# Optimization experiments

Hardware: AMD Instinct MI355X
Metric: run time of the kernel (lower is better)

Reference implementation:

```python
import jax, jax.numpy as jnp
import numpy as np
from jax import lax

B, L, H, V, INNER = 16, 2048, 512, 32000, 8
LR = 0.01
EPS = 1e-5
STD = 0.02


def setup_inputs() -> dict:
    key = jax.random.key(0)
    ks = jax.random.split(key, 14)
    n = lambda k, shape: (jax.random.normal(k, shape, dtype=jnp.float32) * STD)
    return {
        'seq': jax.random.randint(ks[0], (B, L), 0, V, dtype=jnp.int64),
        'embed': n(ks[1], (V, H)),
        'enc_w1': n(ks[2], (2 * H, H)), 'enc_b1': jnp.zeros((2 * H,), jnp.float32),
        'enc_w2': n(ks[3], (H, 2 * H)), 'enc_b2': jnp.zeros((H,), jnp.float32),
        'ln_w': jnp.ones((H,), jnp.float32), 'ln_b': jnp.zeros((H,), jnp.float32),
        'mlp_w1': n(ks[4], (INNER, H)), 'mlp_b1': jnp.zeros((INNER,), jnp.float32),
        'mlp_w2': n(ks[5], (H, INNER)), 'mlp_b2': jnp.zeros((H,), jnp.float32),
        'out_w': n(ks[6], (V, H)), 'out_b': jnp.zeros((V,), jnp.float32),
    }


def _encoder(seq, embed, enc_w1, enc_b1, enc_w2, enc_b2, ln_w, ln_b):
    h = embed[seq]                                        # [B,L,H]
    ff = jax.nn.relu(h @ enc_w1.T + enc_b1) @ enc_w2.T + enc_b2
    x = h + ff
    mu = jnp.mean(x, axis=-1, keepdims=True)
    var = jnp.mean(jnp.square(x - mu), axis=-1, keepdims=True)  # biased, as torch LayerNorm
    return (x - mu) * lax.rsqrt(var + EPS) * ln_w + ln_b


def _inner_mlp(w1, b1, w2, b2, x):
    return w2 @ jax.nn.relu(w1 @ x + b1) + b2


def _ttt_contexts(hidden, mlp_w1, mlp_b1, mlp_w2, mlp_b2):
    # torch detaches hidden and copies base_mlp weights: no grads flow here
    hidden = lax.stop_gradient(hidden)
    p0 = tuple(lax.stop_gradient(p) for p in (mlp_w1, mlp_b1, mlp_w2, mlp_b2))
    ts = np.arange(0, L - 3, 2)                           # 1023 sequential steps
    keys = hidden[:, ts]                                  # [B,T,H]
    vals = hidden[:, ts + 1]                              # [B,T,H]
    query = hidden[:, -1]                                 # [B,H]

    def step(p, kv):
        w1, b1, w2, b2 = p
        k, v = kv
        def loss(w1, b1, w2, b2):
            pred = _inner_mlp(w1, b1, w2, b2, k)
            return jnp.mean(jnp.square(pred - v))
        g1, gb1, g2, gb2 = jax.grad(loss, argnums=(0, 1, 2, 3))(w1, b1, w2, b2)
        return (w1 - LR * g1, b1 - LR * gb1, w2 - LR * g2, b2 - LR * gb2), None

    def run(kb, vb, qb):
        (w1, b1, w2, b2), _ = lax.scan(step, p0, (kb, vb))
        return _inner_mlp(w1, b1, w2, b2, qb)

    return jax.vmap(run)(keys, vals, query)               # [B,H]


def reference(seq, embed, enc_w1, enc_b1, enc_w2, enc_b2, ln_w, ln_b,
              mlp_w1, mlp_b1, mlp_w2, mlp_b2, out_w, out_b):
    hidden = _encoder(seq, embed, enc_w1, enc_b1, enc_w2, enc_b2, ln_w, ln_b)
    ctx = _ttt_contexts(hidden, mlp_w1, mlp_b1, mlp_w2, mlp_b2)
    return ctx @ out_w.T + out_b                          # [B,V]
```

## Files before the change

### kernel.cpp

```cpp
#include <hip/hip_runtime.h>

#define GAS __attribute__((address_space(1)))
#define LAS __attribute__((address_space(3)))

typedef __attribute__((ext_vector_type(8))) short bf16x8;
typedef __attribute__((ext_vector_type(4))) float f32x4;
typedef __attribute__((ext_vector_type(2))) float f32x2;

static constexpr int Bb = 16, Ll = 2048, Hh = 512, Vv = 32000, H2 = 1024;
static constexpr int Mtot = Bb * Ll;
static constexpr float LRc = 0.01f, EPSc = 1e-5f;

static constexpr size_t OFF_X    = 0;
static constexpr size_t OFF_EBF  = OFF_X   + (size_t)Mtot * Hh * 4;
static constexpr size_t OFF_W1BF = OFF_EBF + (size_t)Vv * Hh * 2;
static constexpr size_t OFF_W2BF = OFF_W1BF + (size_t)H2 * Hh * 2;
static constexpr size_t OFF_CTX  = OFF_W2BF + (size_t)Hh * H2 * 2;
static constexpr size_t OFF_FF1  = OFF_CTX + (size_t)Bb * Hh * 4;

__device__ inline unsigned short f2bf(float f) {
  unsigned u = __float_as_uint(f);
  return (unsigned short)((u + 0x7fffu + ((u >> 16) & 1u)) >> 16);
}

__device__ inline f32x2 pk_fma(f32x2 a, f32x2 b, f32x2 c) {
  f32x2 d;
  asm("v_pk_fma_f32 %0, %1, %2, %3" : "=v"(d) : "v"(a), "v"(b), "v"(c));
  return d;
}

#define DPP_ADD(ctrl)                                                        \
  {                                                                          \
    int t_ = __builtin_amdgcn_update_dpp(0, v_, ctrl, 0xf, 0xf, true);       \
    v_ = __float_as_int(__int_as_float(v_) + __int_as_float(t_));            \
  }
__device__ inline float wsum_bcast(float x) {
  int v_ = __float_as_int(x);
  DPP_ADD(0x111)
  DPP_ADD(0x112)
  DPP_ADD(0x114)
  DPP_ADD(0x118)
  DPP_ADD(0x142)
  DPP_ADD(0x143)
  return __int_as_float(__builtin_amdgcn_readlane(v_, 63));
}

__global__ __launch_bounds__(256) void cvt_bf16_kernel(const float* __restrict__ src,
                                                       unsigned short* __restrict__ dst, int n8) {
  int stride = gridDim.x * blockDim.x;
  for (int i = blockIdx.x * blockDim.x + threadIdx.x; i < n8; i += stride) {
    const float4* p = (const float4*)(src + (size_t)i * 8);
    float4 a = p[0], b = p[1];
    uint4 o;
    o.x = f2bf(a.x) | ((unsigned)f2bf(a.y) << 16);
    o.y = f2bf(a.z) | ((unsigned)f2bf(a.w) << 16);
    o.z = f2bf(b.x) | ((unsigned)f2bf(b.y) << 16);
    o.w = f2bf(b.z) | ((unsigned)f2bf(b.w) << 16);
    *(uint4*)(dst + (size_t)i * 8) = o;
  }
}

template <int KTOT, bool GATHER, bool RELUOUT>
__global__ __launch_bounds__(256) void gemm_bt(const unsigned short* __restrict__ Abase,
                                               const int* __restrict__ seq, int seq_off,
                                               const unsigned short* __restrict__ Bmat,
                                               const float* __restrict__ bias,
                                               unsigned short* __restrict__ outb,
                                               float* __restrict__ outf,
                                               int out_row_off, int ldout) {
  __shared__ unsigned short As[128 * 32];
  __shared__ unsigned short Bs[128 * 32];
  __shared__ unsigned long long aoff[128];
  const int tid = threadIdx.x;
  const int m0 = blockIdx.x * 128, n0 = blockIdx.y * 128;

  if (tid < 128) {
    long long r;
    if (GATHER) r = (long long)seq[seq_off + m0 + tid] * KTOT;
    else        r = (long long)(m0 + tid) * KTOT;
    aoff[tid] = (unsigned long long)r;
  }
  __syncthreads();

  const int srow = tid >> 2;
  const int scol = (tid & 3) * 8;
  const int wave = tid >> 6;
  const int lane = tid & 63;
  const int wr = wave >> 1, wc = wave & 1;
  const int fr = lane & 15;
  const int fk = (lane >> 4) * 8;

  f32x4 acc[4][4] = {};

  for (int k0 = 0; k0 < KTOT; k0 += 32) {
#pragma unroll
    for (int i = 0; i < 2; ++i) {
      const unsigned short* ga = Abase + aoff[i * 64 + srow] + k0 + scol;
      __builtin_amdgcn_global_load_lds((const GAS void*)ga,
          (LAS void*)((char*)As + i * 4096 + wave * 1024), 16, 0, 0);
      const unsigned short* gb = Bmat + (size_t)(n0 + i * 64 + srow) * KTOT + k0 + scol;
      __builtin_amdgcn_global_load_lds((const GAS void*)gb,
          (LAS void*)((char*)Bs + i * 4096 + wave * 1024), 16, 0, 0);
    }
    __syncthreads();
    bf16x8 af[4], bfr[4];
#pragma unroll
    for (int m = 0; m < 4; ++m)
      af[m] = *(const bf16x8*)&As[(wr * 64 + m * 16 + fr) * 32 + fk];
#pragma unroll
    for (int n = 0; n < 4; ++n)
      bfr[n] = *(const bf16x8*)&Bs[(wc * 64 + n * 16 + fr) * 32 + fk];
#pragma unroll
    for (int m = 0; m < 4; ++m)
#pragma unroll
      for (int n = 0; n < 4; ++n)
        acc[m][n] = __builtin_amdgcn_mfma_f32_16x16x32_bf16(af[m], bfr[n], acc[m][n], 0, 0, 0);
    __syncthreads();
  }

  float bv[4];
#pragma unroll
  for (int n = 0; n < 4; ++n) bv[n] = bias[n0 + wc * 64 + n * 16 + fr];
#pragma unroll
  for (int m = 0; m < 4; ++m) {
#pragma unroll
    for (int n = 0; n < 4; ++n) {
#pragma unroll
      for (int j = 0; j < 4; ++j) {
        int rl = wr * 64 + m * 16 + ((lane >> 4) << 2) + j;
        int col = n0 + wc * 64 + n * 16 + fr;
        float v = acc[m][n][j] + bv[n];
        size_t off = (size_t)(out_row_off + m0 + rl) * ldout + col;
        if (RELUOUT) { v = fmaxf(v, 0.f); outb[off] = f2bf(v); }
        else outf[off] = v;
      }
    }
  }
}

__global__ __launch_bounds__(256) void ln_kernel(float* __restrict__ xbuf,
                                                 const float* __restrict__ embed,
                                                 const int* __restrict__ seq,
                                                 const float* __restrict__ lnw,
                                                 const float* __restrict__ lnb) {
  int row = blockIdx.x * 4 + (threadIdx.x >> 6);
  int lane = threadIdx.x & 63;
  int c = lane * 8;
  int s = seq[row];
  float* xr = xbuf + (size_t)row * Hh;
  const float* hr = embed + (size_t)s * Hh;
  float4 f0 = *(const float4*)(xr + c), f1 = *(const float4*)(xr + c + 4);
  float4 h0 = *(const float4*)(hr + c), h1 = *(const float4*)(hr + c + 4);
  float x[8] = {f0.x + h0.x, f0.y + h0.y, f0.z + h0.z, f0.w + h0.w,
                f1.x + h1.x, f1.y + h1.y, f1.z + h1.z, f1.w + h1.w};
  float sm = 0.f, sq = 0.f;
#pragma unroll
  for (int u = 0; u < 8; ++u) { sm += x[u]; sq += x[u] * x[u]; }
#pragma unroll
  for (int m = 1; m < 64; m <<= 1) { sm += __shfl_xor(sm, m, 64); sq += __shfl_xor(sq, m, 64); }
  float mu = sm * (1.f / 512.f);
  float var = sq * (1.f / 512.f) - mu * mu;
  float rs = rsqrtf(var + EPSc);
  float y[8];
#pragma unroll
  for (int u = 0; u < 8; ++u) y[u] = (x[u] - mu) * rs * lnw[c + u] + lnb[c + u];
  *(float4*)(xr + c) = make_float4(y[0], y[1], y[2], y[3]);
  *(float4*)(xr + c + 4) = make_float4(y[4], y[5], y[6], y[7]);
}

__global__ __launch_bounds__(64, 1) void ttt_kernel(const float* __restrict__ hidden,
                                                    const float* __restrict__ w1_0,
                                                    const float* __restrict__ b1_0,
                                                    const float* __restrict__ w2_0,
                                                    const float* __restrict__ b2_0,
                                                    float* __restrict__ ctx) {
  const int b = blockIdx.x;
  const int l = threadIdx.x;
  const int c0 = l * 8;
  const float* hb = hidden + (size_t)b * Ll * Hh;
  const float scale = 2.0f / 512.0f;

  f32x2 W1v[8][4];
  f32x2 W2v[8][4];
  float B1[8], B2[8];
#pragma unroll
  for (int j = 0; j < 8; ++j) {
    float4 a = *(const float4*)(w1_0 + (size_t)j * Hh + c0);
    float4 d = *(const float4*)(w1_0 + (size_t)j * Hh + c0 + 4);
    W1v[j][0] = f32x2{a.x, a.y}; W1v[j][1] = f32x2{a.z, a.w};
    W1v[j][2] = f32x2{d.x, d.y}; W1v[j][3] = f32x2{d.z, d.w};
    B1[j] = b1_0[j];
  }
#pragma unroll
  for (int u = 0; u < 8; ++u) {
    float4 a = *(const float4*)(w2_0 + (size_t)(c0 + u) * 8);
    float4 d = *(const float4*)(w2_0 + (size_t)(c0 + u) * 8 + 4);
    W2v[u][0] = f32x2{a.x, a.y}; W2v[u][1] = f32x2{a.z, a.w};
    W2v[u][2] = f32x2{d.x, d.y}; W2v[u][3] = f32x2{d.z, d.w};
  }
  {
    float4 e = *(const float4*)(b2_0 + c0);
    float4 f = *(const float4*)(b2_0 + c0 + 4);
    B2[0] = e.x; B2[1] = e.y; B2[2] = e.z; B2[3] = e.w;
    B2[4] = f.x; B2[5] = f.y; B2[6] = f.z; B2[7] = f.w;
  }

  f32x2 Kc[4];
  float Vs[8];
  const float* pk = hb + c0;
  const float* pv = hb + Hh + c0;
  {
    float4 a = *(const float4*)pk, d = *(const float4*)(pk + 4);
    Kc[0] = f32x2{a.x, a.y}; Kc[1] = f32x2{a.z, a.w};
    Kc[2] = f32x2{d.x, d.y}; Kc[3] = f32x2{d.z, d.w};
    float4 e = *(const float4*)pv, f = *(const float4*)(pv + 4);
    Vs[0] = e.x; Vs[1] = e.y; Vs[2] = e.z; Vs[3] = e.w;
    Vs[4] = f.x; Vs[5] = f.y; Vs[6] = f.z; Vs[7] = f.w;
  }

#pragma unroll 2
  for (int t = 0; t < 1023; ++t) {
    float4 ka, kb, va, vb;
    const bool pre = (t < 1022);
    if (pre) {
      ka = *(const float4*)(pk + 1024); kb = *(const float4*)(pk + 1028);
      va = *(const float4*)(pv + 1024); vb = *(const float4*)(pv + 1028);
    }

    float z[8], h[8];
#pragma unroll
    for (int j = 0; j < 8; ++j) {
      f32x2 acc = {0.f, 0.f};
#pragma unroll
      for (int p = 0; p < 4; ++p) acc = pk_fma(W1v[j][p], Kc[p], acc);
      float s = wsum_bcast(acc.x + acc.y);
      z[j] = s + B1[j];
      h[j] = fmaxf(z[j], 0.f);
    }
    f32x2 h2[4];
#pragma unroll
    for (int p = 0; p < 4; ++p) h2[p] = f32x2{h[2 * p], h[2 * p + 1]};

    float d_[8];
    f32x2 dd[8];
#pragma unroll
    for (int u = 0; u < 8; ++u) {
      f32x2 acc = {0.f, 0.f};
#pragma unroll
      for (int p = 0; p < 4; ++p) acc = pk_fma(W2v[u][p], h2[p], acc);
      float pred = acc.x + acc.y + B2[u];
      float dv = (pred - Vs[u]) * scale;
      d_[u] = dv;
      dd[u] = f32x2{dv, dv};
    }

    f32x2 dhp[4] = {{0.f, 0.f}, {0.f, 0.f}, {0.f, 0.f}, {0.f, 0.f}};
#pragma unroll
    for (int u = 0; u < 8; ++u)
#pragma unroll
      for (int p = 0; p < 4; ++p) dhp[p] = pk_fma(W2v[u][p], dd[u], dhp[p]);
    float dz[8];
#pragma unroll
    for (int p = 0; p < 4; ++p) {
      float s0 = wsum_bcast(dhp[p].x);
      float s1 = wsum_bcast(dhp[p].y);
      dz[2 * p]     = (z[2 * p]     > 0.f) ? s0 : 0.f;
      dz[2 * p + 1] = (z[2 * p + 1] > 0.f) ? s1 : 0.f;
    }

#pragma unroll
    for (int u = 0; u < 8; ++u) {
      float g = -LRc * d_[u];
      f32x2 gv = {g, g};
#pragma unroll
      for (int p = 0; p < 4; ++p) W2v[u][p] = pk_fma(gv, h2[p], W2v[u][p]);
      B2[u] = fmaf(-LRc, d_[u], B2[u]);
    }
#pragma unroll
    for (int j = 0; j < 8; ++j) {
      float g = -LRc * dz[j];
      f32x2 gv = {g, g};
#pragma unroll
      for (int p = 0; p < 4; ++p) W1v[j][p] = pk_fma(gv, Kc[p], W1v[j][p]);
      B1[j] = fmaf(-LRc, dz[j], B1[j]);
    }

    if (pre) {
      Kc[0] = f32x2{ka.x, ka.y}; Kc[1] = f32x2{ka.z, ka.w};
      Kc[2] = f32x2{kb.x, kb.y}; Kc[3] = f32x2{kb.z, kb.w};
      Vs[0] = va.x; Vs[1] = va.y; Vs[2] = va.z; Vs[3] = va.w;
      Vs[4] = vb.x; Vs[5] = vb.y; Vs[6] = vb.z; Vs[7] = vb.w;
      pk += 1024; pv += 1024;
    }
  }

  {
    const float* pq = hb + (size_t)(Ll - 1) * Hh + c0;
    float4 a = *(const float4*)pq, d = *(const float4*)(pq + 4);
    f32x2 Q[4] = {f32x2{a.x, a.y}, f32x2{a.z, a.w}, f32x2{d.x, d.y}, f32x2{d.z, d.w}};
    float h[8];
#pragma unroll
    for (int j = 0; j < 8; ++j) {
      f32x2 acc = {0.f, 0.f};
#pragma unroll
      for (int p = 0; p < 4; ++p) acc = pk_fma(W1v[j][p], Q[p], acc);
      float s = wsum_bcast(acc.x + acc.y);
      h[j] = fmaxf(s + B1[j], 0.f);
    }
    f32x2 h2[4];
#pragma unroll
    for (int p = 0; p < 4; ++p) h2[p] = f32x2{h[2 * p], h[2 * p + 1]};
    float o[8];
#pragma unroll
    for (int u = 0; u < 8; ++u) {
      f32x2 acc = {0.f, 0.f};
#pragma unroll
      for (int p = 0; p < 4; ++p) acc = pk_fma(W2v[u][p], h2[p], acc);
      o[u] = acc.x + acc.y + B2[u];
    }
    float* cp = ctx + (size_t)b * Hh + c0;
    *(float4*)cp = make_float4(o[0], o[1], o[2], o[3]);
    *(float4*)(cp + 4) = make_float4(o[4], o[5], o[6], o[7]);
  }
}

__global__ __launch_bounds__(256) void out_kernel(const float* __restrict__ ctx,
                                                  const float* __restrict__ outw,
                                                  const float* __restrict__ outb_,
                                                  float* __restrict__ out) {
  __shared__ float cs[16 * 516];
  int tid = threadIdx.x;
#pragma unroll
  for (int r = 0; r < 32; ++r) {
    int idx = r * 256 + tid;
    cs[(idx >> 9) * 516 + (idx & 511)] = ctx[idx];
  }
  __syncthreads();
  int v = blockIdx.x * 16 + (tid >> 4);
  int b = tid & 15;
  const float4* wr = (const float4*)(outw + (size_t)v * 512);
  const float4* cr = (const float4*)(cs + b * 516);
  float acc = 0.f;
#pragma unroll 8
  for (int k = 0; k < 128; ++k) {
    float4 wv = wr[k];
    float4 cv = cr[k];
    acc += wv.x * cv.x + wv.y * cv.y + wv.z * cv.z + wv.w * cv.w;
  }
  out[(size_t)b * 32000 + v] = acc + outb_[v];
}

extern "C" void kernel_launch(void* const* d_in, const int* in_sizes, int n_in,
                              void* d_out, int out_size, void* d_ws, size_t ws_size,
                              hipStream_t stream) {
  const int*   seq    = (const int*)d_in[0];
  const float* embed  = (const float*)d_in[1];
  const float* enc_w1 = (const float*)d_in[2];
  const float* enc_b1 = (const float*)d_in[3];
  const float* enc_w2 = (const float*)d_in[4];
  const float* enc_b2 = (const float*)d_in[5];
  const float* ln_w   = (const float*)d_in[6];
  const float* ln_b   = (const float*)d_in[7];
  const float* mlp_w1 = (const float*)d_in[8];
  const float* mlp_b1 = (const float*)d_in[9];
  const float* mlp_w2 = (const float*)d_in[10];
  const float* mlp_b2 = (const float*)d_in[11];
  const float* out_w  = (const float*)d_in[12];
  const float* out_b  = (const float*)d_in[13];
  float* out = (float*)d_out;

  char* ws = (char*)d_ws;
  float*          xbuf = (float*)(ws + OFF_X);
  unsigned short* ebf  = (unsigned short*)(ws + OFF_EBF);
  unsigned short* w1bf = (unsigned short*)(ws + OFF_W1BF);
  unsigned short* w2bf = (unsigned short*)(ws + OFF_W2BF);
  float*          ctx  = (float*)(ws + OFF_CTX);
  unsigned short* ff1  = (unsigned short*)(ws + OFF_FF1);

  const int cand[4] = {1, 2, 4, 8};
  int nc = 8;
  for (int ci = 0; ci < 4; ++ci) {
    if (OFF_FF1 + (size_t)(Mtot / cand[ci]) * H2 * 2 <= ws_size) { nc = cand[ci]; break; }
  }

  cvt_bf16_kernel<<<2048, 256, 0, stream>>>(embed, ebf, Vv * Hh / 8);
  cvt_bf16_kernel<<<256, 256, 0, stream>>>(enc_w1, w1bf, H2 * Hh / 8);
  cvt_bf16_kernel<<<256, 256, 0, stream>>>(enc_w2, w2bf, Hh * H2 / 8);

  const int Mc = Mtot / nc;
  for (int c = 0; c < nc; ++c) {
    const int m0 = c * Mc;
    gemm_bt<512, true, true><<<dim3(Mc / 128, 8), 256, 0, stream>>>(
        ebf, seq, m0, w1bf, enc_b1, ff1, nullptr, 0, H2);
    gemm_bt<1024, false, false><<<dim3(Mc / 128, 4), 256, 0, stream>>>(
        ff1, nullptr, 0, w2bf, enc_b2, nullptr, xbuf, m0, Hh);
  }
  ln_kernel<<<Mtot / 4, 256, 0, stream>>>(xbuf, embed, seq, ln_w, ln_b);
  ttt_kernel<<<Bb, 64, 0, stream>>>(xbuf, mlp_w1, mlp_b1, mlp_w2, mlp_b2, ctx);
  out_kernel<<<Vv / 16, 256, 0, stream>>>(ctx, out_w, out_b, out);
}
```

Measured before the change: 1.017 ms.

## Precompute next-step hidden pre-activation algebraically to shorten the TTT serial chain

Reformulates the sequential TTT scan so the next step's first-layer pre-activation is computed from the old W1 applied to the next key, plus a rank-1 correction using the key dot product (kap+1) and dz. This takes the W1·k reduction off the critical dependency chain after the weight update, letting it overlap with the backward pass. The key dot product adds one extra wave reduction per step. Prefetching now always reads rows 2t+3 and 2t+4 without the guard, which reads past the last used key at the final step (still in bounds of the hidden buffer). The unroll factor also changes from 2 to 3.

```diff
diff --git a/kernel.cpp b/kernel.cpp
--- a/kernel.cpp
+++ b/kernel.cpp
@@ -182,14 +182,15 @@
 
   f32x2 W1v[8][4];
   f32x2 W2v[8][4];
-  float B1[8], B2[8];
+  float B1u[8];
+  float B2[8];
 #pragma unroll
   for (int j = 0; j < 8; ++j) {
     float4 a = *(const float4*)(w1_0 + (size_t)j * Hh + c0);
     float4 d = *(const float4*)(w1_0 + (size_t)j * Hh + c0 + 4);
     W1v[j][0] = f32x2{a.x, a.y}; W1v[j][1] = f32x2{a.z, a.w};
     W1v[j][2] = f32x2{d.x, d.y}; W1v[j][3] = f32x2{d.z, d.w};
-    B1[j] = b1_0[j];
+    B1u[j] = b1_0[j];
   }
 #pragma unroll
   for (int u = 0; u < 8; ++u) {
@@ -205,41 +206,68 @@
     B2[4] = f.x; B2[5] = f.y; B2[6] = f.z; B2[7] = f.w;
   }
 
-  f32x2 Kc[4];
+  f32x2 Kc[4], Kn[4];
   float Vs[8];
-  const float* pk = hb + c0;
-  const float* pv = hb + Hh + c0;
   {
-    float4 a = *(const float4*)pk, d = *(const float4*)(pk + 4);
+    const float* p0 = hb + c0;
+    float4 a = *(const float4*)p0, d = *(const float4*)(p0 + 4);
     Kc[0] = f32x2{a.x, a.y}; Kc[1] = f32x2{a.z, a.w};
     Kc[2] = f32x2{d.x, d.y}; Kc[3] = f32x2{d.z, d.w};
-    float4 e = *(const float4*)pv, f = *(const float4*)(pv + 4);
-    Vs[0] = e.x; Vs[1] = e.y; Vs[2] = e.z; Vs[3] = e.w;
-    Vs[4] = f.x; Vs[5] = f.y; Vs[6] = f.z; Vs[7] = f.w;
-  }
-
-#pragma unroll 2
+    const float* p1 = hb + 2 * Hh + c0;
+    float4 e = *(const float4*)p1, f = *(const float4*)(p1 + 4);
+    Kn[0] = f32x2{e.x, e.y}; Kn[1] = f32x2{e.z, e.w};
+    Kn[2] = f32x2{f.x, f.y}; Kn[3] = f32x2{f.z, f.w};
+    const float* pv = hb + Hh + c0;
+    float4 g = *(const float4*)pv, h4 = *(const float4*)(pv + 4);
+    Vs[0] = g.x; Vs[1] = g.y; Vs[2] = g.z; Vs[3] = g.w;
+    Vs[4] = h4.x; Vs[5] = h4.y; Vs[6] = h4.z; Vs[7] = h4.w;
+  }
+
+  float zu[8];
+#pragma unroll
+  for (int j = 0; j < 8; ++j) {
+    f32x2 acc = {0.f, 0.f};
+#pragma unroll
+    for (int p = 0; p < 4; ++p) acc = pk_fma(W1v[j][p], Kc[p], acc);
+    zu[j] = wsum_bcast(acc.x + acc.y) + B1u[j];
+  }
+
+#pragma unroll 3
   for (int t = 0; t < 1023; ++t) {
     float4 ka, kb, va, vb;
-    const bool pre = (t < 1022);
-    if (pre) {
-      ka = *(const float4*)(pk + 1024); kb = *(const float4*)(pk + 1028);
-      va = *(const float4*)(pv + 1024); vb = *(const float4*)(pv + 1028);
-    }
-
-    float z[8], h[8];
+    {
+      const float* pf = hb + (size_t)(2 * t + 4) * Hh + c0;
+      ka = *(const float4*)pf; kb = *(const float4*)(pf + 4);
+      const float* pv = hb + (size_t)(2 * t + 3) * Hh + c0;
+      va = *(const float4*)pv; vb = *(const float4*)(pv + 4);
+    }
+
+    float kap;
+    {
+      f32x2 acc = {0.f, 0.f};
+#pragma unroll
+      for (int p = 0; p < 4; ++p) acc = pk_fma(Kc[p], Kn[p], acc);
+      kap = wsum_bcast(acc.x + acc.y);
+    }
+    float ys[8];
 #pragma unroll
     for (int j = 0; j < 8; ++j) {
       f32x2 acc = {0.f, 0.f};
 #pragma unroll
-      for (int p = 0; p < 4; ++p) acc = pk_fma(W1v[j][p], Kc[p], acc);
-      float s = wsum_bcast(acc.x + acc.y);
-      z[j] = s + B1[j];
-      h[j] = fmaxf(z[j], 0.f);
-    }
+      for (int p = 0; p < 4; ++p) acc = pk_fma(W1v[j][p], Kn[p], acc);
+      ys[j] = wsum_bcast(acc.x + acc.y);
+    }
+
+    float hu[8];
+#pragma unroll
+    for (int j = 0; j < 8; ++j) hu[j] = fmaxf(zu[j], 0.f);
     f32x2 h2[4];
 #pragma unroll
-    for (int p = 0; p < 4; ++p) h2[p] = f32x2{h[2 * p], h[2 * p + 1]};
+    for (int p = 0; p < 4; ++p) h2[p] = f32x2{hu[2 * p], hu[2 * p + 1]};
+    const f32x2 nlr = {-LRc, -LRc};
+    f32x2 nh2[4];
+#pragma unroll
+    for (int p = 0; p < 4; ++p) nh2[p] = h2[p] * nlr;
 
     float d_[8];
     f32x2 dd[8];
@@ -259,21 +287,24 @@
     for (int u = 0; u < 8; ++u)
 #pragma unroll
       for (int p = 0; p < 4; ++p) dhp[p] = pk_fma(W2v[u][p], dd[u], dhp[p]);
+
     float dz[8];
 #pragma unroll
     for (int p = 0; p < 4; ++p) {
       float s0 = wsum_bcast(dhp[p].x);
       float s1 = wsum_bcast(dhp[p].y);
-      dz[2 * p]     = (z[2 * p]     > 0.f) ? s0 : 0.f;
-      dz[2 * p + 1] = (z[2 * p + 1] > 0.f) ? s1 : 0.f;
-    }
+      dz[2 * p]     = (zu[2 * p]     > 0.f) ? s0 : 0.f;
+      dz[2 * p + 1] = (zu[2 * p + 1] > 0.f) ? s1 : 0.f;
+    }
+
+    float t1 = -LRc * (kap + 1.f);
+#pragma unroll
+    for (int j = 0; j < 8; ++j) zu[j] = (ys[j] + B1u[j]) + t1 * dz[j];
 
 #pragma unroll
     for (int u = 0; u < 8; ++u) {
-      float g = -LRc * d_[u];
-      f32x2 gv = {g, g};
-#pragma unroll
-      for (int p = 0; p < 4; ++p) W2v[u][p] = pk_fma(gv, h2[p], W2v[u][p]);
+#pragma unroll
+      for (int p = 0; p < 4; ++p) W2v[u][p] = pk_fma(dd[u], nh2[p], W2v[u][p]);
       B2[u] = fmaf(-LRc, d_[u], B2[u]);
     }
 #pragma unroll
@@ -282,34 +313,32 @@
       f32x2 gv = {g, g};
 #pragma unroll
       for (int p = 0; p < 4; ++p) W1v[j][p] = pk_fma(gv, Kc[p], W1v[j][p]);
-      B1[j] = fmaf(-LRc, dz[j], B1[j]);
-    }
-
-    if (pre) {
-      Kc[0] = f32x2{ka.x, ka.y}; Kc[1] = f32x2{ka.z, ka.w};
-      Kc[2] = f32x2{kb.x, kb.y}; Kc[3] = f32x2{kb.z, kb.w};
-      Vs[0] = va.x; Vs[1] = va.y; Vs[2] = va.z; Vs[3] = va.w;
-      Vs[4] = vb.x; Vs[5] = vb.y; Vs[6] = vb.z; Vs[7] = vb.w;
-      pk += 1024; pv += 1024;
-    }
+      B1u[j] = fmaf(-LRc, dz[j], B1u[j]);
+    }
+
+#pragma unroll
+    for (int p = 0; p < 4; ++p) Kc[p] = Kn[p];
+    Kn[0] = f32x2{ka.x, ka.y}; Kn[1] = f32x2{ka.z, ka.w};
+    Kn[2] = f32x2{kb.x, kb.y}; Kn[3] = f32x2{kb.z, kb.w};
+    Vs[0] = va.x; Vs[1] = va.y; Vs[2] = va.z; Vs[3] = va.w;
+    Vs[4] = vb.x; Vs[5] = vb.y; Vs[6] = vb.z; Vs[7] = vb.w;
   }
 
   {
     const float* pq = hb + (size_t)(Ll - 1) * Hh + c0;
     float4 a = *(const float4*)pq, d = *(const float4*)(pq + 4);
     f32x2 Q[4] = {f32x2{a.x, a.y}, f32x2{a.z, a.w}, f32x2{d.x, d.y}, f32x2{d.z, d.w}};
-    float h[8];
+    float hq[8];
 #pragma unroll
     for (int j = 0; j < 8; ++j) {
       f32x2 acc = {0.f, 0.f};
 #pragma unroll
       for (int p = 0; p < 4; ++p) acc = pk_fma(W1v[j][p], Q[p], acc);
-      float s = wsum_bcast(acc.x + acc.y);
-      h[j] = fmaxf(s + B1[j], 0.f);
+      hq[j] = fmaxf(wsum_bcast(acc.x + acc.y) + B1u[j], 0.f);
     }
     f32x2 h2[4];
 #pragma unroll
-    for (int p = 0; p < 4; ++p) h2[p] = f32x2{h[2 * p], h[2 * p + 1]};
+    for (int p = 0; p < 4; ++p) h2[p] = f32x2{hq[2 * p], hq[2 * p + 1]};
     float o[8];
 #pragma unroll
     for (int u = 0; u < 8; ++u) {
```

Result: slower. 1.069 ms (+5.0%).
